# Kernel tuning notes

Hardware: AMD Instinct MI355X
Metric: run time of the kernel (lower is better)

Reference implementation:

```python
import jax, jax.numpy as jnp
import numpy as np

N_NODES = 100000
E_ORIG = 600000   # entries in edge_dict_original -> nodes of second stage
E_LINE = 1200000  # edges among edge-nodes
H = 128
OUT = 64
BN_EPS = 1e-5
N_LAYERS = 2  # num_initial_gin_layers == num_gin_layers == 2


def setup_inputs() -> dict:
    key = jax.random.key(0)
    ks = iter(jax.random.split(key, 64))
    def nrm(shape, s=0.05):
        return jax.random.normal(next(ks), shape, jnp.float32) * s
    inp = {}
    inp["edge_index"] = jax.random.randint(next(ks), (2, E_LINE), 0, E_ORIG)
    inp["x_original"] = jax.random.normal(next(ks), (N_NODES, H), jnp.float32)
    inp["edge_index_original"] = jax.random.randint(next(ks), (2, E_ORIG), 0, N_NODES)
    inp["edge_pairs"] = jax.random.randint(next(ks), (E_ORIG, 2), 0, N_NODES)
    for pfx in ("init", "gin"):
        inp[pfx + "_W1"] = nrm((N_LAYERS, H, H))
        inp[pfx + "_b1"] = nrm((N_LAYERS, H))
        inp[pfx + "_g"] = jnp.ones((N_LAYERS, H), jnp.float32) + nrm((N_LAYERS, H))
        inp[pfx + "_bb"] = nrm((N_LAYERS, H))
        inp[pfx + "_m"] = nrm((N_LAYERS, H))
        inp[pfx + "_v"] = jnp.ones((N_LAYERS, H), jnp.float32) + jax.random.uniform(next(ks), (N_LAYERS, H), jnp.float32) * 0.1
        inp[pfx + "_W2"] = nrm((N_LAYERS, H, H))
        inp[pfx + "_b2"] = nrm((N_LAYERS, H))
    inp["mlp_W1"] = nrm((H, H)); inp["mlp_b1"] = nrm((H,))
    inp["mlp_g"] = jnp.ones((H,), jnp.float32) + nrm((H,))
    inp["mlp_bb"] = nrm((H,)); inp["mlp_m"] = nrm((H,))
    inp["mlp_v"] = jnp.ones((H,), jnp.float32) + jax.random.uniform(next(ks), (H,), jnp.float32) * 0.1
    inp["mlp_W2"] = nrm((H, H)); inp["mlp_b2"] = nrm((H,))
    inp["out_W"] = nrm((H, OUT)); inp["out_b"] = nrm((OUT,))
    return inp


def _bn(h, g, b, m, v):  # eval-mode BatchNorm1d
    return (h - m) * jax.lax.rsqrt(v + BN_EPS) * g + b


def _gin_conv(x, ei, n, W1, b1, g, bb, m, v, W2, b2):
    # GINConv (eps=0): nn(x + sum_{j in N(i)} x_j)
    agg = jax.ops.segment_sum(x[ei[0]], ei[1], num_segments=n)
    h = x + agg
    h = jax.nn.relu(_bn(h @ W1 + b1, g, bb, m, v))
    return jax.nn.relu(h @ W2 + b2)


def reference(edge_index, x_original, edge_index_original, edge_pairs,
              init_W1, init_b1, init_g, init_bb, init_m, init_v, init_W2, init_b2,
              mlp_W1, mlp_b1, mlp_g, mlp_bb, mlp_m, mlp_v, mlp_W2, mlp_b2,
              gin_W1, gin_b1, gin_g, gin_bb, gin_m, gin_v, gin_W2, gin_b2,
              out_W, out_b):
    x = x_original
    for i in range(N_LAYERS):  # initial GIN layers on original graph (dropout=eval identity)
        x = _gin_conv(x, edge_index_original, N_NODES,
                      init_W1[i], init_b1[i], init_g[i], init_bb[i], init_m[i], init_v[i],
                      init_W2[i], init_b2[i])
    # per-edge gather of node pairs; concat-then-split == two gathers
    def mlp(h):  # PyG MLP, 2 layers, plain last
        h = jax.nn.relu(_bn(h @ mlp_W1 + mlp_b1, mlp_g, mlp_bb, mlp_m, mlp_v))
        return h @ mlp_W2 + mlp_b2
    h = mlp(x[edge_pairs[:, 0]]) + mlp(x[edge_pairs[:, 1]])  # [E_ORIG, H]
    for i in range(N_LAYERS):  # GIN layers on edge-node graph
        h = _gin_conv(h, edge_index, E_ORIG,
                      gin_W1[i], gin_b1[i], gin_g[i], gin_bb[i], gin_m[i], gin_v[i],
                      gin_W2[i], gin_b2[i])
    return h @ out_W + out_b  # [E_ORIG, OUT]
```

## Files before the change

### kernel.cpp

```cpp
#include <hip/hip_runtime.h>
#include <hip/hip_bf16.h>

typedef __bf16 bf8_t __attribute__((ext_vector_type(8)));
typedef float  f32x4 __attribute__((ext_vector_type(4)));

constexpr int N_NODES = 100000;
constexpr int E_ORIG  = 600000;
constexpr int E_LINE  = 1200000;

static inline int cdiv(int a, int b) { return (a + b - 1) / b; }

enum { A_DENSE = 0, A_AGG = 1, A_PAIR = 2 };

__global__ void k_f2b(const float* __restrict__ X, __bf16* __restrict__ O, int n8) {
    int i = blockIdx.x * 256 + threadIdx.x;
    if (i >= n8) return;
    float4 a = ((const float4*)X)[2 * i], b = ((const float4*)X)[2 * i + 1];
    bf8_t o;
    o[0] = (__bf16)a.x; o[1] = (__bf16)a.y; o[2] = (__bf16)a.z; o[3] = (__bf16)a.w;
    o[4] = (__bf16)b.x; o[5] = (__bf16)b.y; o[6] = (__bf16)b.z; o[7] = (__bf16)b.w;
    ((bf8_t*)O)[i] = o;
}

__global__ void k_hist(const int* __restrict__ dst, int* __restrict__ cnt, int E) {
    int e = blockIdx.x * 256 + threadIdx.x;
    if (e < E) atomicAdd(&cnt[dst[e]], 1);
}

__global__ void k_scan1(const int* __restrict__ cnt, int* __restrict__ offs,
                        int* __restrict__ bsum, int n) {
    __shared__ int tmp[256];
    int i = blockIdx.x * 256 + threadIdx.x;
    int v = (i < n) ? cnt[i] : 0;
    tmp[threadIdx.x] = v; __syncthreads();
    #pragma unroll
    for (int d = 1; d < 256; d <<= 1) {
        int t = (threadIdx.x >= d) ? tmp[threadIdx.x - d] : 0;
        __syncthreads();
        tmp[threadIdx.x] += t;
        __syncthreads();
    }
    if (i < n) offs[i] = tmp[threadIdx.x] - v;
    if (threadIdx.x == 255) bsum[blockIdx.x] = tmp[255];
}

__global__ void k_scan2(int* __restrict__ bsum, int nb) {
    __shared__ int tmp[256];
    __shared__ int carry;
    if (threadIdx.x == 0) carry = 0;
    __syncthreads();
    for (int base = 0; base < nb; base += 256) {
        int i = base + threadIdx.x;
        int v = (i < nb) ? bsum[i] : 0;
        tmp[threadIdx.x] = v; __syncthreads();
        #pragma unroll
        for (int d = 1; d < 256; d <<= 1) {
            int t = (threadIdx.x >= d) ? tmp[threadIdx.x - d] : 0;
            __syncthreads();
            tmp[threadIdx.x] += t;
            __syncthreads();
        }
        int tot = tmp[255];
        if (i < nb) bsum[i] = tmp[threadIdx.x] - v + carry;
        __syncthreads();
        if (threadIdx.x == 0) carry += tot;
        __syncthreads();
    }
}

__global__ void k_scan3(int* __restrict__ offs, int* __restrict__ cur,
                        const int* __restrict__ bsum, int n) {
    int i = blockIdx.x * 256 + threadIdx.x;
    if (i >= n) return;
    int o = offs[i] + bsum[blockIdx.x];
    offs[i] = o;
    cur[i]  = o;
}

__global__ void k_fill(const int* __restrict__ src, const int* __restrict__ dst,
                       int* __restrict__ cur, int* __restrict__ adj, int E) {
    int e = blockIdx.x * 256 + threadIdx.x;
    if (e >= E) return;
    int p = atomicAdd(&cur[dst[e]], 1);
    adj[p] = src[e];
}

struct WPtrs { const float* p[10]; };

__global__ void k_packW(WPtrs wp, __bf16* __restrict__ out) {
    const float* W = wp.p[blockIdx.x];
    __bf16* O = out + (size_t)blockIdx.x * 16384;
    const float4* W4 = (const float4*)W;
    for (int e = threadIdx.x; e < 4096; e += 256) {
        float4 w = W4[e];
        unsigned flat = (unsigned)e * 4;
        unsigned k = flat >> 7, n = flat & 127;
        unsigned c = n >> 4, s = k >> 5, hi = (k >> 3) & 3, j = k & 7;
        unsigned l0 = (hi << 4) | (n & 15);
        unsigned base = ((c * 4 + s) * 64 + l0) * 8 + j;
        O[base]      = (__bf16)w.x;
        O[base + 8]  = (__bf16)w.y;
        O[base + 16] = (__bf16)w.z;
        O[base + 24] = (__bf16)w.w;
    }
}

template<int MODE, bool RELU2>
__launch_bounds__(256, 2)
__global__ void k_layer(const __bf16* __restrict__ X, int M,
                        const int* __restrict__ offs, const int* __restrict__ cnt,
                        const int* __restrict__ adj, const int* __restrict__ pairs,
                        const __bf16* __restrict__ Wp1, const __bf16* __restrict__ Wp2,
                        const float* __restrict__ b1,
                        const float* __restrict__ bg, const float* __restrict__ bb,
                        const float* __restrict__ bm, const float* __restrict__ bv,
                        const float* __restrict__ b2,
                        __bf16* __restrict__ out) {
    __shared__ __bf16 sA[128 * 128];
    __shared__ __bf16 sW[128 * 128];
    __shared__ float sS1[128], sT1[128], sT2[128];

    const int tid = threadIdx.x;
    const int rowBase = blockIdx.x * 128;

    bf8_t w1r[8];
    #pragma unroll
    for (int i = 0; i < 8; ++i) w1r[i] = ((const bf8_t*)Wp1)[i * 256 + tid];

    if (tid < 128) {
        float b = b1[tid];
        float g = bg[tid], be = bb[tid], m = bm[tid], v = bv[tid];
        float S = g * rsqrtf(v + 1e-5f);
        sS1[tid] = S;
        sT1[tid] = b * S + (be - m * S);
        sT2[tid] = b2[tid];
    }

    if (MODE != A_DENSE) {
        const int c  = tid & 15;
        const int r0 = tid >> 4;
        for (int p = 0; p < 8; ++p) {
            int rl = p * 16 + r0;
            int grow = rowBase + rl;
            float acc[8];
            if (grow < M) {
                int s = offs[grow], n = cnt[grow];
                if (MODE == A_AGG) {
                    bf8_t self = *((const bf8_t*)(X + (size_t)grow * 128) + c);
                    #pragma unroll
                    for (int j = 0; j < 8; ++j) acc[j] = (float)self[j];
                    int k = 0;
                    for (; k + 2 <= n; k += 2) {
                        int a0 = adj[s + k], a1 = adj[s + k + 1];
                        bf8_t v0 = *((const bf8_t*)(X + (size_t)a0 * 128) + c);
                        bf8_t v1 = *((const bf8_t*)(X + (size_t)a1 * 128) + c);
                        #pragma unroll
                        for (int j = 0; j < 8; ++j) acc[j] += (float)v0[j];
                        #pragma unroll
                        for (int j = 0; j < 8; ++j) acc[j] += (float)v1[j];
                    }
                    if (k < n) {
                        int a0 = adj[s + k];
                        bf8_t v0 = *((const bf8_t*)(X + (size_t)a0 * 128) + c);
                        #pragma unroll
                        for (int j = 0; j < 8; ++j) acc[j] += (float)v0[j];
                    }
                } else {
                    int2 pr = ((const int2*)pairs)[grow];
                    bf8_t v0 = *((const bf8_t*)(X + (size_t)pr.x * 128) + c);
                    bf8_t v1 = *((const bf8_t*)(X + (size_t)pr.y * 128) + c);
                    #pragma unroll
                    for (int j = 0; j < 8; ++j) acc[j] = (float)v0[j] + (float)v1[j];
                    int k = 0;
                    for (; k + 2 <= n; k += 2) {
                        int a0 = adj[s + k], a1 = adj[s + k + 1];
                        int2 q0 = ((const int2*)pairs)[a0];
                        int2 q1 = ((const int2*)pairs)[a1];
                        bf8_t u0 = *((const bf8_t*)(X + (size_t)q0.x * 128) + c);
                        bf8_t u1 = *((const bf8_t*)(X + (size_t)q0.y * 128) + c);
                        bf8_t u2 = *((const bf8_t*)(X + (size_t)q1.x * 128) + c);
                        bf8_t u3 = *((const bf8_t*)(X + (size_t)q1.y * 128) + c);
                        #pragma unroll
                        for (int j = 0; j < 8; ++j)
                            acc[j] += (float)u0[j] + (float)u1[j] + (float)u2[j] + (float)u3[j];
                    }
                    if (k < n) {
                        int a0 = adj[s + k];
                        int2 q0 = ((const int2*)pairs)[a0];
                        bf8_t u0 = *((const bf8_t*)(X + (size_t)q0.x * 128) + c);
                        bf8_t u1 = *((const bf8_t*)(X + (size_t)q0.y * 128) + c);
                        #pragma unroll
                        for (int j = 0; j < 8; ++j) acc[j] += (float)u0[j] + (float)u1[j];
                    }
                }
            } else {
                #pragma unroll
                for (int j = 0; j < 8; ++j) acc[j] = 0.f;
            }
            bf8_t o;
            #pragma unroll
            for (int j = 0; j < 8; ++j) o[j] = (__bf16)acc[j];
            *(bf8_t*)&sA[rl * 128 + ((c ^ (rl & 7)) << 3)] = o;
        }
    }

    #pragma unroll
    for (int i = 0; i < 8; ++i) ((bf8_t*)sW)[i * 256 + tid] = w1r[i];
    __syncthreads();

    bf8_t w2r[8];
    #pragma unroll
    for (int i = 0; i < 8; ++i) w2r[i] = ((const bf8_t*)Wp2)[i * 256 + tid];

    const int lane = tid & 63;
    const int wv   = tid >> 6;
    const int m0 = lane & 15, kq = lane >> 4;

    f32x4 acc[2][8];
    #pragma unroll
    for (int rt = 0; rt < 2; ++rt)
        #pragma unroll
        for (int ct = 0; ct < 8; ++ct) acc[rt][ct] = (f32x4){0.f, 0.f, 0.f, 0.f};

    #pragma unroll
    for (int s = 0; s < 4; ++s) {
        bf8_t fa[2];
        #pragma unroll
        for (int rt = 0; rt < 2; ++rt) {
            int rl = wv * 32 + rt * 16 + m0;
            if (MODE == A_DENSE) {
                int r = rowBase + rl;
                r = r < M ? r : M - 1;
                fa[rt] = *(const bf8_t*)(X + (size_t)r * 128 + s * 32 + kq * 8);
            } else {
                int chunk = s * 4 + kq;
                fa[rt] = *(const bf8_t*)&sA[rl * 128 + ((chunk ^ (rl & 7)) << 3)];
            }
        }
        #pragma unroll
        for (int ct = 0; ct < 8; ++ct) {
            bf8_t fw = *(const bf8_t*)&sW[((ct * 4 + s) * 64 + lane) * 8];
            #pragma unroll
            for (int rt = 0; rt < 2; ++rt)
                acc[rt][ct] = __builtin_amdgcn_mfma_f32_16x16x32_bf16(fa[rt], fw, acc[rt][ct], 0, 0, 0);
        }
    }

    #pragma unroll
    for (int rt = 0; rt < 2; ++rt) {
        #pragma unroll
        for (int r = 0; r < 4; ++r) {
            int rl = wv * 32 + rt * 16 + kq * 4 + r;
            #pragma unroll
            for (int ct = 0; ct < 8; ++ct) {
                int col = ct * 16 + m0;
                float v = acc[rt][ct][r] * sS1[col] + sT1[col];
                v = fmaxf(v, 0.f);
                int chunk = col >> 3;
                sA[rl * 128 + ((chunk ^ (rl & 7)) << 3) + (col & 7)] = (__bf16)v;
            }
        }
    }
    __syncthreads();

    #pragma unroll
    for (int i = 0; i < 8; ++i) ((bf8_t*)sW)[i * 256 + tid] = w2r[i];
    __syncthreads();

    f32x4 acc2[2][8];
    #pragma unroll
    for (int rt = 0; rt < 2; ++rt)
        #pragma unroll
        for (int ct = 0; ct < 8; ++ct) acc2[rt][ct] = (f32x4){0.f, 0.f, 0.f, 0.f};

    #pragma unroll
    for (int s = 0; s < 4; ++s) {
        bf8_t fa[2];
        #pragma unroll
        for (int rt = 0; rt < 2; ++rt) {
            int rl = wv * 32 + rt * 16 + m0;
            int chunk = s * 4 + kq;
            fa[rt] = *(const bf8_t*)&sA[rl * 128 + ((chunk ^ (rl & 7)) << 3)];
        }
        #pragma unroll
        for (int ct = 0; ct < 8; ++ct) {
            bf8_t fw = *(const bf8_t*)&sW[((ct * 4 + s) * 64 + lane) * 8];
            #pragma unroll
            for (int rt = 0; rt < 2; ++rt)
                acc2[rt][ct] = __builtin_amdgcn_mfma_f32_16x16x32_bf16(fa[rt], fw, acc2[rt][ct], 0, 0, 0);
        }
    }

    #pragma unroll
    for (int rt = 0; rt < 2; ++rt) {
        #pragma unroll
        for (int r = 0; r < 4; ++r) {
            int row = rowBase + wv * 32 + rt * 16 + kq * 4 + r;
            if (row < M) {
                #pragma unroll
                for (int ct = 0; ct < 8; ++ct) {
                    int col = ct * 16 + m0;
                    float v = acc2[rt][ct][r] + sT2[col];
                    if (RELU2) v = fmaxf(v, 0.f);
                    out[(size_t)row * 128 + col] = (__bf16)v;
                }
            }
        }
    }
}

template<int NC, bool BN, bool RELU, bool OUTF32>
__launch_bounds__(256, 2)
__global__ void k_gemm(const __bf16* __restrict__ A, int M,
                       const float* __restrict__ W,
                       const float* __restrict__ bias,
                       const float* __restrict__ bg, const float* __restrict__ bb,
                       const float* __restrict__ bm, const float* __restrict__ bv,
                       void* __restrict__ outp) {
    constexpr int NT = NC / 16;
    __shared__ __bf16 sW[128 * NC];
    __shared__ float sS[NC];
    __shared__ float sT[NC];

    const float4* W4 = (const float4*)W;
    for (int e = threadIdx.x; e < 32 * NC; e += 256) {
        float4 w = W4[e];
        unsigned flat = (unsigned)e * 4;
        unsigned k = flat / NC, n = flat % NC;
        unsigned c = n >> 4, s = k >> 5, hi = (k >> 3) & 3, j = k & 7;
        unsigned l0 = (hi << 4) | (n & 15);
        unsigned base = ((c * 4 + s) * 64 + l0) * 8 + j;
        sW[base]      = (__bf16)w.x;
        sW[base + 8]  = (__bf16)w.y;
        sW[base + 16] = (__bf16)w.z;
        sW[base + 24] = (__bf16)w.w;
    }
    for (int n = threadIdx.x; n < NC; n += 256) {
        float b = bias[n];
        float S = 1.0f, T = b;
        if (BN) {
            float g = bg[n], be = bb[n], m = bm[n], v = bv[n];
            S = g * rsqrtf(v + 1e-5f);
            T = b * S + (be - m * S);
        }
        sS[n] = S; sT[n] = T;
    }
    __syncthreads();

    const int lane = threadIdx.x & 63;
    const int wv   = threadIdx.x >> 6;
    const int rowBase = blockIdx.x * 256 + wv * 64;
    const int m0 = lane & 15, kq = lane >> 4;

    f32x4 acc[4][NT];
    #pragma unroll
    for (int rt = 0; rt < 4; ++rt)
        #pragma unroll
        for (int ct = 0; ct < NT; ++ct)
            acc[rt][ct] = (f32x4){0.f, 0.f, 0.f, 0.f};

    #pragma unroll
    for (int s = 0; s < 4; ++s) {
        bf8_t fa[4];
        #pragma unroll
        for (int rt = 0; rt < 4; ++rt) {
            int r = rowBase + rt * 16 + m0;
            r = r < M ? r : M - 1;
            fa[rt] = *(const bf8_t*)(A + (size_t)r * 128 + s * 32 + kq * 8);
        }
        #pragma unroll
        for (int ct = 0; ct < NT; ++ct) {
            bf8_t fw = *(const bf8_t*)&sW[((ct * 4 + s) * 64 + lane) * 8];
            #pragma unroll
            for (int rt = 0; rt < 4; ++rt)
                acc[rt][ct] = __builtin_amdgcn_mfma_f32_16x16x32_bf16(fa[rt], fw, acc[rt][ct], 0, 0, 0);
        }
    }

    #pragma unroll
    for (int rt = 0; rt < 4; ++rt) {
        #pragma unroll
        for (int r = 0; r < 4; ++r) {
            int row = rowBase + rt * 16 + kq * 4 + r;
            if (row < M) {
                #pragma unroll
                for (int ct = 0; ct < NT; ++ct) {
                    int col = ct * 16 + m0;
                    float v = acc[rt][ct][r] * sS[col] + sT[col];
                    if (RELU) v = fmaxf(v, 0.0f);
                    size_t o = (size_t)row * NC + col;
                    if constexpr (OUTF32) ((float*)outp)[o]  = v;
                    else                  ((__bf16*)outp)[o] = (__bf16)v;
                }
            }
        }
    }
}

extern "C" void kernel_launch(void* const* d_in, const int* in_sizes, int n_in,
                              void* d_out, int out_size, void* d_ws, size_t ws_size,
                              hipStream_t stream) {
    const int*   edge_index = (const int*)d_in[0];
    const float* x_orig     = (const float*)d_in[1];
    const int*   eio        = (const int*)d_in[2];
    const int*   pairs      = (const int*)d_in[3];
    const float* iW1 = (const float*)d_in[4];
    const float* ib1 = (const float*)d_in[5];
    const float* ig  = (const float*)d_in[6];
    const float* ibb = (const float*)d_in[7];
    const float* im  = (const float*)d_in[8];
    const float* iv  = (const float*)d_in[9];
    const float* iW2 = (const float*)d_in[10];
    const float* ib2 = (const float*)d_in[11];
    const float* gW1 = (const float*)d_in[12];
    const float* gb1 = (const float*)d_in[13];
    const float* gg  = (const float*)d_in[14];
    const float* gbb = (const float*)d_in[15];
    const float* gm  = (const float*)d_in[16];
    const float* gv  = (const float*)d_in[17];
    const float* gW2 = (const float*)d_in[18];
    const float* gb2 = (const float*)d_in[19];
    const float* mW1 = (const float*)d_in[20];
    const float* mb1 = (const float*)d_in[21];
    const float* mg  = (const float*)d_in[22];
    const float* mbb = (const float*)d_in[23];
    const float* mm  = (const float*)d_in[24];
    const float* mv  = (const float*)d_in[25];
    const float* mW2 = (const float*)d_in[26];
    const float* mb2 = (const float*)d_in[27];
    const float* oW  = (const float*)d_in[28];
    const float* ob  = (const float*)d_in[29];

    char* w = (char*)d_ws;
    __bf16* EB  = (__bf16*)w;                w += (size_t)E_ORIG * 128 * 2;
    __bf16* XB  = (__bf16*)w;                w += (size_t)N_NODES * 128 * 2;
    __bf16* NA  = (__bf16*)w;                w += (size_t)N_NODES * 128 * 2;
    __bf16* NB  = (__bf16*)w;                w += (size_t)N_NODES * 128 * 2;
    int* cnt  = (int*)w;                     w += (size_t)E_ORIG * 4;
    int* offs = (int*)w;                     w += (size_t)E_ORIG * 4;
    int* cur  = (int*)w;                     w += (size_t)E_ORIG * 4;
    int* bsum = (int*)w;                     w += 4096 * 4;
    int* adj  = (int*)w;                     w += (size_t)E_LINE * 4;
    __bf16* Wpk = (__bf16*)w;
    __bf16* EBd = (__bf16*)d_out;

    const int* eio_src = eio;
    const int* eio_dst = eio + E_ORIG;
    const int* el_src  = edge_index;
    const int* el_dst  = edge_index + E_LINE;

    const int nBlk = cdiv(N_NODES, 128);
    const int eBlk = cdiv(E_ORIG, 128);
    const int nScanNB = cdiv(N_NODES, 256);
    const int eScanNB = cdiv(E_ORIG, 256);

    WPtrs wp;
    wp.p[0] = iW1;          wp.p[1] = iW2;
    wp.p[2] = iW1 + 16384;  wp.p[3] = iW2 + 16384;
    wp.p[4] = mW1;          wp.p[5] = mW2;
    wp.p[6] = gW1;          wp.p[7] = gW2;
    wp.p[8] = gW1 + 16384;  wp.p[9] = gW2 + 16384;
    k_packW<<<10, 256, 0, stream>>>(wp, Wpk);

    hipMemsetAsync(cnt, 0, (size_t)N_NODES * 4, stream);
    k_hist <<<cdiv(E_ORIG, 256), 256, 0, stream>>>(eio_dst, cnt, E_ORIG);
    k_scan1<<<nScanNB, 256, 0, stream>>>(cnt, offs, bsum, N_NODES);
    k_scan2<<<1, 256, 0, stream>>>(bsum, nScanNB);
    k_scan3<<<nScanNB, 256, 0, stream>>>(offs, cur, bsum, N_NODES);
    k_fill <<<cdiv(E_ORIG, 256), 256, 0, stream>>>(eio_src, eio_dst, cur, adj, E_ORIG);

    k_f2b<<<cdiv(N_NODES * 16, 256), 256, 0, stream>>>(x_orig, XB, N_NODES * 16);
    k_layer<A_AGG, true><<<nBlk, 256, 0, stream>>>(XB, N_NODES, offs, cnt, adj, nullptr,
        Wpk + 0 * 16384, Wpk + 1 * 16384, ib1, ig, ibb, im, iv, ib2, NA);
    k_layer<A_AGG, true><<<nBlk, 256, 0, stream>>>(NA, N_NODES, offs, cnt, adj, nullptr,
        Wpk + 2 * 16384, Wpk + 3 * 16384, ib1 + 128, ig + 128, ibb + 128, im + 128, iv + 128, ib2 + 128, NB);
    k_layer<A_DENSE, false><<<nBlk, 256, 0, stream>>>(NB, N_NODES, nullptr, nullptr, nullptr, nullptr,
        Wpk + 4 * 16384, Wpk + 5 * 16384, mb1, mg, mbb, mm, mv, mb2, XB);

    hipMemsetAsync(cnt, 0, (size_t)E_ORIG * 4, stream);
    k_hist <<<cdiv(E_LINE, 256), 256, 0, stream>>>(el_dst, cnt, E_LINE);
    k_scan1<<<eScanNB, 256, 0, stream>>>(cnt, offs, bsum, E_ORIG);
    k_scan2<<<1, 256, 0, stream>>>(bsum, eScanNB);
    k_scan3<<<eScanNB, 256, 0, stream>>>(offs, cur, bsum, E_ORIG);
    k_fill <<<cdiv(E_LINE, 256), 256, 0, stream>>>(el_src, el_dst, cur, adj, E_LINE);

    k_layer<A_PAIR, true><<<eBlk, 256, 0, stream>>>(XB, E_ORIG, offs, cnt, adj, pairs,
        Wpk + 6 * 16384, Wpk + 7 * 16384, gb1, gg, gbb, gm, gv, gb2, EBd);
    k_layer<A_AGG, true><<<eBlk, 256, 0, stream>>>(EBd, E_ORIG, offs, cnt, adj, nullptr,
        Wpk + 8 * 16384, Wpk + 9 * 16384, gb1 + 128, gg + 128, gbb + 128, gm + 128, gv + 128, gb2 + 128, EB);

    k_gemm<64, false, false, true><<<cdiv(E_ORIG, 256), 256, 0, stream>>>(EB, E_ORIG, oW, ob,
        nullptr, nullptr, nullptr, nullptr, d_out);
}
```

Before: 1.311 ms.

## Drop shared weight tile, batch first-neighbor gathers, raise occupancy to four blocks

```diff
diff --git a/kernel.cpp b/kernel.cpp
--- a/kernel.cpp
+++ b/kernel.cpp
@@ -106,7 +106,7 @@
 }
 
 template<int MODE, bool RELU2>
-__launch_bounds__(256, 2)
+__launch_bounds__(256, 4)
 __global__ void k_layer(const __bf16* __restrict__ X, int M,
                         const int* __restrict__ offs, const int* __restrict__ cnt,
                         const int* __restrict__ adj, const int* __restrict__ pairs,
@@ -117,47 +117,64 @@
                         const float* __restrict__ b2,
                         __bf16* __restrict__ out) {
     __shared__ __bf16 sA[128 * 128];
-    __shared__ __bf16 sW[128 * 128];
-    __shared__ float sS1[128], sT1[128], sT2[128];
-
-    const int tid = threadIdx.x;
+
+    const int tid  = threadIdx.x;
+    const int lane = tid & 63;
+    const int wv   = tid >> 6;
     const int rowBase = blockIdx.x * 128;
-
-    bf8_t w1r[8];
-    #pragma unroll
-    for (int i = 0; i < 8; ++i) w1r[i] = ((const bf8_t*)Wp1)[i * 256 + tid];
-
-    if (tid < 128) {
-        float b = b1[tid];
-        float g = bg[tid], be = bb[tid], m = bm[tid], v = bv[tid];
-        float S = g * rsqrtf(v + 1e-5f);
-        sS1[tid] = S;
-        sT1[tid] = b * S + (be - m * S);
-        sT2[tid] = b2[tid];
-    }
+    const int m0 = lane & 15, kq = lane >> 4;
 
     if (MODE != A_DENSE) {
-        const int c  = tid & 15;
-        const int r0 = tid >> 4;
+        const int c    = lane & 15;
+        const int slot = lane >> 4;
+        int sarr[8], narr[8];
+        #pragma unroll
         for (int p = 0; p < 8; ++p) {
-            int rl = p * 16 + r0;
-            int grow = rowBase + rl;
-            float acc[8];
-            if (grow < M) {
-                int s = offs[grow], n = cnt[grow];
-                if (MODE == A_AGG) {
-                    bf8_t self = *((const bf8_t*)(X + (size_t)grow * 128) + c);
+            int grow = rowBase + wv * 32 + p * 4 + slot;
+            int g = grow < M ? grow : 0;
+            sarr[p] = offs[g];
+            narr[p] = grow < M ? cnt[g] : 0;
+        }
+        int pa0[8], pa1[8];
+        #pragma unroll
+        for (int p = 0; p < 8; ++p) {
+            pa0[p] = narr[p] > 0 ? adj[sarr[p]]     : 0;
+            pa1[p] = narr[p] > 1 ? adj[sarr[p] + 1] : 0;
+        }
+
+        if (MODE == A_AGG) {
+            #pragma unroll
+            for (int half = 0; half < 2; ++half) {
+                bf8_t sv[4], n0[4], n1[4];
+                #pragma unroll
+                for (int q = 0; q < 4; ++q) {
+                    int p = half * 4 + q;
+                    int grow = rowBase + wv * 32 + p * 4 + slot;
+                    int g = grow < M ? grow : 0;
+                    sv[q] = *((const bf8_t*)(X + (size_t)g      * 128) + c);
+                    n0[q] = *((const bf8_t*)(X + (size_t)pa0[p] * 128) + c);
+                    n1[q] = *((const bf8_t*)(X + (size_t)pa1[p] * 128) + c);
+                }
+                #pragma unroll
+                for (int q = 0; q < 4; ++q) {
+                    int p = half * 4 + q;
+                    int rl = wv * 32 + p * 4 + slot;
+                    int n = narr[p];
+                    float acc[8];
                     #pragma unroll
-                    for (int j = 0; j < 8; ++j) acc[j] = (float)self[j];
-                    int k = 0;
+                    for (int j = 0; j < 8; ++j) {
+                        float a = (float)sv[q][j];
+                        if (n > 0) a += (float)n0[q][j];
+                        if (n > 1) a += (float)n1[q][j];
+                        acc[j] = a;
+                    }
+                    int s = sarr[p], k = 2;
                     for (; k + 2 <= n; k += 2) {
                         int a0 = adj[s + k], a1 = adj[s + k + 1];
                         bf8_t v0 = *((const bf8_t*)(X + (size_t)a0 * 128) + c);
                         bf8_t v1 = *((const bf8_t*)(X + (size_t)a1 * 128) + c);
                         #pragma unroll
-                        for (int j = 0; j < 8; ++j) acc[j] += (float)v0[j];
-                        #pragma unroll
-                        for (int j = 0; j < 8; ++j) acc[j] += (float)v1[j];
+                        for (int j = 0; j < 8; ++j) acc[j] += (float)v0[j] + (float)v1[j];
                     }
                     if (k < n) {
                         int a0 = adj[s + k];
@@ -165,56 +182,61 @@
                         #pragma unroll
                         for (int j = 0; j < 8; ++j) acc[j] += (float)v0[j];
                     }
-                } else {
-                    int2 pr = ((const int2*)pairs)[grow];
-                    bf8_t v0 = *((const bf8_t*)(X + (size_t)pr.x * 128) + c);
-                    bf8_t v1 = *((const bf8_t*)(X + (size_t)pr.y * 128) + c);
+                    bf8_t o;
                     #pragma unroll
-                    for (int j = 0; j < 8; ++j) acc[j] = (float)v0[j] + (float)v1[j];
-                    int k = 0;
-                    for (; k + 2 <= n; k += 2) {
-                        int a0 = adj[s + k], a1 = adj[s + k + 1];
-                        int2 q0 = ((const int2*)pairs)[a0];
-                        int2 q1 = ((const int2*)pairs)[a1];
-                        bf8_t u0 = *((const bf8_t*)(X + (size_t)q0.x * 128) + c);
-                        bf8_t u1 = *((const bf8_t*)(X + (size_t)q0.y * 128) + c);
-                        bf8_t u2 = *((const bf8_t*)(X + (size_t)q1.x * 128) + c);
-                        bf8_t u3 = *((const bf8_t*)(X + (size_t)q1.y * 128) + c);
+                    for (int j = 0; j < 8; ++j) o[j] = (__bf16)acc[j];
+                    *(bf8_t*)&sA[rl * 128 + ((c ^ (rl & 7)) << 3)] = o;
+                }
+            }
+        } else {
+            #pragma unroll
+            for (int half = 0; half < 2; ++half) {
+                int2 spr[4], pq0[4], pq1[4];
+                #pragma unroll
+                for (int q = 0; q < 4; ++q) {
+                    int p = half * 4 + q;
+                    int grow = rowBase + wv * 32 + p * 4 + slot;
+                    int g = grow < M ? grow : 0;
+                    spr[q] = ((const int2*)pairs)[g];
+                    pq0[q] = ((const int2*)pairs)[pa0[p]];
+                    pq1[q] = ((const int2*)pairs)[pa1[p]];
+                }
+                #pragma unroll
+                for (int q = 0; q < 4; ++q) {
+                    int p = half * 4 + q;
+                    int rl = wv * 32 + p * 4 + slot;
+                    int n = narr[p];
+                    bf8_t s0 = *((const bf8_t*)(X + (size_t)spr[q].x * 128) + c);
+                    bf8_t s1 = *((const bf8_t*)(X + (size_t)spr[q].y * 128) + c);
+                    bf8_t u0 = *((const bf8_t*)(X + (size_t)pq0[q].x * 128) + c);
+                    bf8_t u1 = *((const bf8_t*)(X + (size_t)pq0[q].y * 128) + c);
+                    bf8_t u2 = *((const bf8_t*)(X + (size_t)pq1[q].x * 128) + c);
+                    bf8_t u3 = *((const bf8_t*)(X + (size_t)pq1[q].y * 128) + c);
+                    float acc[8];
+                    #pragma unroll
+                    for (int j = 0; j < 8; ++j) {
+                        float a = (float)s0[j] + (float)s1[j];
+                        if (n > 0) a += (float)u0[j] + (float)u1[j];
+                        if (n > 1) a += (float)u2[j] + (float)u3[j];
+                        acc[j] = a;
+                    }
+                    int s = sarr[p];
+                    for (int k = 2; k < n; ++k) {
+                        int a0 = adj[s + k];
+                        int2 qq = ((const int2*)pairs)[a0];
+                        bf8_t w0 = *((const bf8_t*)(X + (size_t)qq.x * 128) + c);
+                        bf8_t w1 = *((const bf8_t*)(X + (size_t)qq.y * 128) + c);
                         #pragma unroll
-                        for (int j = 0; j < 8; ++j)
-                            acc[j] += (float)u0[j] + (float)u1[j] + (float)u2[j] + (float)u3[j];
+                        for (int j = 0; j < 8; ++j) acc[j] += (float)w0[j] + (float)w1[j];
                     }
-                    if (k < n) {
-                        int a0 = adj[s + k];
-                        int2 q0 = ((const int2*)pairs)[a0];
-                        bf8_t u0 = *((const bf8_t*)(X + (size_t)q0.x * 128) + c);
-                        bf8_t u1 = *((const bf8_t*)(X + (size_t)q0.y * 128) + c);
-                        #pragma unroll
-                        for (int j = 0; j < 8; ++j) acc[j] += (float)u0[j] + (float)u1[j];
-                    }
+                    bf8_t o;
+                    #pragma unroll
+                    for (int j = 0; j < 8; ++j) o[j] = (__bf16)acc[j];
+                    *(bf8_t*)&sA[rl * 128 + ((c ^ (rl & 7)) << 3)] = o;
                 }
-            } else {
-                #pragma unroll
-                for (int j = 0; j < 8; ++j) acc[j] = 0.f;
             }
-            bf8_t o;
-            #pragma unroll
-            for (int j = 0; j < 8; ++j) o[j] = (__bf16)acc[j];
-            *(bf8_t*)&sA[rl * 128 + ((c ^ (rl & 7)) << 3)] = o;
-        }
-    }
-
-    #pragma unroll
-    for (int i = 0; i < 8; ++i) ((bf8_t*)sW)[i * 256 + tid] = w1r[i];
-    __syncthreads();
-
-    bf8_t w2r[8];
-    #pragma unroll
-    for (int i = 0; i < 8; ++i) w2r[i] = ((const bf8_t*)Wp2)[i * 256 + tid];
-
-    const int lane = tid & 63;
-    const int wv   = tid >> 6;
-    const int m0 = lane & 15, kq = lane >> 4;
+        }
+    }
 
     f32x4 acc[2][8];
     #pragma unroll
@@ -239,11 +261,23 @@
         }
         #pragma unroll
         for (int ct = 0; ct < 8; ++ct) {
-            bf8_t fw = *(const bf8_t*)&sW[((ct * 4 + s) * 64 + lane) * 8];
+            bf8_t fw = *(const bf8_t*)(Wp1 + ((size_t)((ct * 4 + s) * 64 + lane)) * 8);
             #pragma unroll
             for (int rt = 0; rt < 2; ++rt)
                 acc[rt][ct] = __builtin_amdgcn_mfma_f32_16x16x32_bf16(fa[rt], fw, acc[rt][ct], 0, 0, 0);
         }
+    }
+
+    float S1r[8], T1r[8], T2r[8];
+    #pragma unroll
+    for (int ct = 0; ct < 8; ++ct) {
+        int col = ct * 16 + m0;
+        float b = b1[col];
+        float g = bg[col], be = bb[col], m_ = bm[col], v_ = bv[col];
+        float S = g * rsqrtf(v_ + 1e-5f);
+        S1r[ct] = S;
+        T1r[ct] = b * S + (be - m_ * S);
+        T2r[ct] = b2[col];
     }
 
     #pragma unroll
@@ -254,18 +288,13 @@
             #pragma unroll
             for (int ct = 0; ct < 8; ++ct) {
                 int col = ct * 16 + m0;
-                float v = acc[rt][ct][r] * sS1[col] + sT1[col];
+                float v = acc[rt][ct][r] * S1r[ct] + T1r[ct];
                 v = fmaxf(v, 0.f);
                 int chunk = col >> 3;
                 sA[rl * 128 + ((chunk ^ (rl & 7)) << 3) + (col & 7)] = (__bf16)v;
             }
         }
     }
-    __syncthreads();
-
-    #pragma unroll
-    for (int i = 0; i < 8; ++i) ((bf8_t*)sW)[i * 256 + tid] = w2r[i];
-    __syncthreads();
 
     f32x4 acc2[2][8];
     #pragma unroll
@@ -284,7 +313,7 @@
         }
         #pragma unroll
         for (int ct = 0; ct < 8; ++ct) {
-            bf8_t fw = *(const bf8_t*)&sW[((ct * 4 + s) * 64 + lane) * 8];
+            bf8_t fw = *(const bf8_t*)(Wp2 + ((size_t)((ct * 4 + s) * 64 + lane)) * 8);
             #pragma unroll
             for (int rt = 0; rt < 2; ++rt)
                 acc2[rt][ct] = __builtin_amdgcn_mfma_f32_16x16x32_bf16(fa[rt], fw, acc2[rt][ct], 0, 0, 0);
@@ -300,7 +329,7 @@
                 #pragma unroll
                 for (int ct = 0; ct < 8; ++ct) {
                     int col = ct * 16 + m0;
-                    float v = acc2[rt][ct][r] + sT2[col];
+                    float v = acc2[rt][ct][r] + T2r[ct];
                     if (RELU2) v = fmaxf(v, 0.f);
                     out[(size_t)row * 128 + col] = (__bf16)v;
                 }
```

Result: faster. 1.082 ms (-17.5%).
